# Kernel tuning notes

Measured on AMD Instinct MI355X. Metric: run time of the kernel, lower is better.

## Reference

```python
import jax, jax.numpy as jnp
import numpy as np

MIN_C, MAX_C = 1e-4, 1e4
EPS_C = 1e-6
TAU = 1.0            # fixed temperature (learnable_temperature=False), clamp is a no-op here
NORM_EPS = 1e-15
ARTANH_EPS = 1e-7

B, C, D = 512, 512, 512


def _expmap0(u, sc):
    # geoopt expmap0 for k = -c: tanh(sqrt(c)*||u||) * u / (sqrt(c)*||u||)
    norm = jnp.maximum(jnp.linalg.norm(u, axis=-1, keepdims=True), NORM_EPS)
    return jnp.tanh(sc * norm) * u / (sc * norm)


def setup_inputs() -> dict:
    key = jax.random.key(0)
    k1, k2 = jax.random.split(key)
    euclidean_feats = jax.random.normal(k1, (B, D), dtype=jnp.float32) * 0.05
    proto_tan = jax.random.normal(k2, (C, D), dtype=jnp.float32) * 0.001  # proto_init_std
    raw_c = jnp.asarray(0.0, dtype=jnp.float32)  # log(init_curvature=1.0)
    return {"euclidean_feats": euclidean_feats, "proto_tan": proto_tan, "raw_c": raw_c}


def reference(euclidean_feats, proto_tan, raw_c):
    # current_c(): softplus(raw_c) + eps, clipped
    c = jnp.clip(jax.nn.softplus(raw_c) + EPS_C, MIN_C, MAX_C)
    sc = jnp.sqrt(c)

    z = _expmap0(euclidean_feats, sc)  # (B, D) points on Poincare ball
    p = _expmap0(proto_tan, sc)        # (C, D)

    # dist(z, p) = 2/sqrt(c) * artanh(sqrt(c) * || (-z) mobius_add p ||)
    x = -z                                      # (B, D)
    x2 = jnp.sum(x * x, axis=-1)[:, None]       # (B, 1)
    y2 = jnp.sum(p * p, axis=-1)[None, :]       # (1, C)
    xy = x @ p.T                                # (B, C) inner products (GEMM)

    # mobius_add with k = -c:
    # num = (1 + 2c<x,y> + c||y||^2) x + (1 - c||x||^2) y
    # den = 1 + 2c<x,y> + c^2 ||x||^2 ||y||^2
    num = ((1.0 + 2.0 * c * xy + c * y2)[..., None] * x[:, None, :]
           + (1.0 - c * x2)[..., None] * p[None, :, :])     # (B, C, D)
    den = jnp.maximum(1.0 + 2.0 * c * xy + (c * c) * x2 * y2, NORM_EPS)  # (B, C)
    m = num / den[..., None]

    mnorm = jnp.linalg.norm(m, axis=-1)  # (B, C)
    t = jnp.clip(sc * mnorm, -1.0 + ARTANH_EPS, 1.0 - ARTANH_EPS)
    d = (2.0 / sc) * jnp.arctanh(t)      # (B, C) hyperbolic distances

    return -d / TAU
```

## Files before the change

kernel.cpp:

```cpp
#include <hip/hip_runtime.h>
#include <math.h>

#define B_ 512
#define C_ 512
#define D_ 512
#define LDK 520

typedef __attribute__((ext_vector_type(8))) short s8v;
typedef __attribute__((ext_vector_type(4))) short s4v;
typedef __attribute__((ext_vector_type(4))) float f4v;

__device__ __forceinline__ float compute_c_dev(float rc) {
    float sp = fmaxf(rc, 0.0f) + log1pf(expf(-fabsf(rc)));
    float c = sp + 1e-6f;
    return fminf(fmaxf(c, 1e-4f), 1e4f);
}

__device__ __forceinline__ unsigned short f2bf(float f) {
    unsigned u = __float_as_uint(f);
    u += 0x7FFFu + ((u >> 16) & 1u);
    return (unsigned short)(u >> 16);
}

__device__ __forceinline__ float dist_val(float zp, float x2, float y2,
                                          float c, float scc, float inv_sc) {
    float xy = -zp;
    float two_cxy = 2.0f * c * xy;
    float a = 1.0f + two_cxy + c * y2;
    float b = 1.0f - c * x2;
    float den = fmaxf(1.0f + two_cxy + c * c * x2 * y2, 1e-15f);
    float num2 = a * a * x2 + 2.0f * a * b * xy + b * b * y2;
    float mn = sqrtf(fmaxf(num2, 0.0f)) / den;
    float t = fminf(scc * mn, 1.0f - 1e-7f);
    return -inv_sc * logf((1.0f + t) / (1.0f - t));
}

__global__ __launch_bounds__(256, 1) void fused_kernel(
    const float* __restrict__ feats, const float* __restrict__ protos,
    const float* __restrict__ raw_c, float* __restrict__ out)
{
    __shared__ short zs[32 * LDK];
    __shared__ short ps[32 * LDK];
    __shared__ float x2s[32];
    __shared__ float y2s[32];

    const int t    = threadIdx.x;
    const int lane = t & 63;
    const int w    = t >> 6;
    const int row0 = blockIdx.y * 32;
    const int col0 = blockIdx.x * 32;

    const float c      = compute_c_dev(raw_c[0]);
    const float scc    = sqrtf(c);
    const float inv_sc = 1.0f / scc;

    {
        const float4* srcA = (const float4*)(feats + (size_t)(row0 + 8 * w) * D_);
        float4 v0[8], v1[8];
        #pragma unroll
        for (int i = 0; i < 8; ++i) {
            v0[i] = srcA[i * 128 + lane];
            v1[i] = srcA[i * 128 + lane + 64];
        }
        #pragma unroll
        for (int i = 0; i < 8; ++i) {
            int r = 8 * w + i;
            float ss = v0[i].x*v0[i].x + v0[i].y*v0[i].y + v0[i].z*v0[i].z + v0[i].w*v0[i].w
                     + v1[i].x*v1[i].x + v1[i].y*v1[i].y + v1[i].z*v1[i].z + v1[i].w*v1[i].w;
            #pragma unroll
            for (int off = 32; off > 0; off >>= 1) ss += __shfl_xor(ss, off);
            float n = fmaxf(sqrtf(ss), 1e-15f);
            float s = tanhf(scc * n) / (scc * n);
            if (lane == 0) x2s[r] = s * s * ss;
            s4v lo, hi;
            lo[0]=(short)f2bf(v0[i].x); lo[1]=(short)f2bf(v0[i].y);
            lo[2]=(short)f2bf(v0[i].z); lo[3]=(short)f2bf(v0[i].w);
            hi[0]=(short)f2bf(v1[i].x); hi[1]=(short)f2bf(v1[i].y);
            hi[2]=(short)f2bf(v1[i].z); hi[3]=(short)f2bf(v1[i].w);
            lo[0]=(short)f2bf(v0[i].x*s); lo[1]=(short)f2bf(v0[i].y*s);
            lo[2]=(short)f2bf(v0[i].z*s); lo[3]=(short)f2bf(v0[i].w*s);
            hi[0]=(short)f2bf(v1[i].x*s); hi[1]=(short)f2bf(v1[i].y*s);
            hi[2]=(short)f2bf(v1[i].z*s); hi[3]=(short)f2bf(v1[i].w*s);
            *(s4v*)(&zs[r * LDK + 4 * lane])       = lo;
            *(s4v*)(&zs[r * LDK + 256 + 4 * lane]) = hi;
        }
    }
    {
        const float4* srcB = (const float4*)(protos + (size_t)(col0 + 8 * w) * D_);
        float4 v0[8], v1[8];
        #pragma unroll
        for (int i = 0; i < 8; ++i) {
            v0[i] = srcB[i * 128 + lane];
            v1[i] = srcB[i * 128 + lane + 64];
        }
        #pragma unroll
        for (int i = 0; i < 8; ++i) {
            int r = 8 * w + i;
            float ss = v0[i].x*v0[i].x + v0[i].y*v0[i].y + v0[i].z*v0[i].z + v0[i].w*v0[i].w
                     + v1[i].x*v1[i].x + v1[i].y*v1[i].y + v1[i].z*v1[i].z + v1[i].w*v1[i].w;
            #pragma unroll
            for (int off = 32; off > 0; off >>= 1) ss += __shfl_xor(ss, off);
            float n = fmaxf(sqrtf(ss), 1e-15f);
            float s = tanhf(scc * n) / (scc * n);
            if (lane == 0) y2s[r] = s * s * ss;
            s4v lo, hi;
            lo[0]=(short)f2bf(v0[i].x*s); lo[1]=(short)f2bf(v0[i].y*s);
            lo[2]=(short)f2bf(v0[i].z*s); lo[3]=(short)f2bf(v0[i].w*s);
            hi[0]=(short)f2bf(v1[i].x*s); hi[1]=(short)f2bf(v1[i].y*s);
            hi[2]=(short)f2bf(v1[i].z*s); hi[3]=(short)f2bf(v1[i].w*s);
            *(s4v*)(&ps[r * LDK + 4 * lane])       = lo;
            *(s4v*)(&ps[r * LDK + 256 + 4 * lane]) = hi;
        }
    }

    __syncthreads();

    const int wr = w >> 1, wc = w & 1;
    const int rowA = 16 * wr + (lane & 15);
    const int rowB = 16 * wc + (lane & 15);
    const short* za = &zs[rowA * LDK + 8 * (lane >> 4)];
    const short* pa = &ps[rowB * LDK + 8 * (lane >> 4)];

    f4v acc = {0.f, 0.f, 0.f, 0.f};
    #pragma unroll
    for (int kk = 0; kk < 16; ++kk) {
        s8v af = *(const s8v*)(za + kk * 32);
        s8v bf = *(const s8v*)(pa + kk * 32);
        acc = __builtin_amdgcn_mfma_f32_16x16x32_bf16(af, bf, acc, 0, 0, 0);
    }

    const int col   = lane & 15;
    const int rbase = 4 * (lane >> 4);
    const int gcol  = col0 + 16 * wc + col;
    const float y2  = y2s[16 * wc + col];
    #pragma unroll
    for (int r = 0; r < 4; ++r) {
        int lrow = 16 * wr + rbase + r;
        float x2 = x2s[lrow];
        out[(size_t)(row0 + lrow) * C_ + gcol] = dist_val(acc[r], x2, y2, c, scc, inv_sc);
    }
}

extern "C" void kernel_launch(void* const* d_in, const int* in_sizes, int n_in,
                              void* d_out, int out_size, void* d_ws, size_t ws_size,
                              hipStream_t stream) {
    const float* feats  = (const float*)d_in[0];
    const float* protos = (const float*)d_in[1];
    const float* raw_c  = (const float*)d_in[2];
    float* out = (float*)d_out;

    dim3 grid(C_ / 32, B_ / 32);
    fused_kernel<<<grid, 256, 0, stream>>>(feats, protos, raw_c, out);
}
```

Before: 66.62 us.

## Double block size, load A/B tiles in parallel, split-K MFMA across wave halves

Raises the block from 256 to 512 threads. Waves 0-3 now load and normalize the feature tile while waves 4-7 handle the prototype tile at the same time, instead of one wave group doing both in sequence. The K dimension of the MFMA loop is split between the two wave halves and reduced through shared memory, which adds one extra barrier. It also switches to fast intrinsics for tanh, division and log, and removes the dead first bf16 conversion pass, trading some accuracy for shorter transcendental paths.

New measurement: 63.62 us. -4.5%, faster.

```diff
diff --git a/kernel.cpp b/kernel.cpp
--- a/kernel.cpp
+++ b/kernel.cpp
@@ -22,6 +22,11 @@
     return (unsigned short)(u >> 16);
 }
 
+__device__ __forceinline__ float fast_tanh_pos(float x) {
+    float e = __expf(2.0f * x);
+    return 1.0f - __fdividef(2.0f, e + 1.0f);
+}
+
 __device__ __forceinline__ float dist_val(float zp, float x2, float y2,
                                           float c, float scc, float inv_sc) {
     float xy = -zp;
@@ -30,12 +35,12 @@
     float b = 1.0f - c * x2;
     float den = fmaxf(1.0f + two_cxy + c * c * x2 * y2, 1e-15f);
     float num2 = a * a * x2 + 2.0f * a * b * xy + b * b * y2;
-    float mn = sqrtf(fmaxf(num2, 0.0f)) / den;
+    float mn = __fdividef(sqrtf(fmaxf(num2, 0.0f)), den);
     float t = fminf(scc * mn, 1.0f - 1e-7f);
-    return -inv_sc * logf((1.0f + t) / (1.0f - t));
+    return -inv_sc * __logf(__fdividef(1.0f + t, 1.0f - t));
 }
 
-__global__ __launch_bounds__(256, 1) void fused_kernel(
+__global__ __launch_bounds__(512, 2) void fused_kernel(
     const float* __restrict__ feats, const float* __restrict__ protos,
     const float* __restrict__ raw_c, float* __restrict__ out)
 {
@@ -43,6 +48,7 @@
     __shared__ short ps[32 * LDK];
     __shared__ float x2s[32];
     __shared__ float y2s[32];
+    __shared__ f4v  accbuf[256];
 
     const int t    = threadIdx.x;
     const int lane = t & 63;
@@ -55,89 +61,74 @@
     const float inv_sc = 1.0f / scc;
 
     {
-        const float4* srcA = (const float4*)(feats + (size_t)(row0 + 8 * w) * D_);
+        const bool  isB = (w >= 4);
+        const int   wl  = isB ? (w - 4) : w;
+        const float* src = isB ? (protos + (size_t)(col0 + 8 * wl) * D_)
+                               : (feats  + (size_t)(row0 + 8 * wl) * D_);
+        short* dst = isB ? ps : zs;
+        float* sqv = isB ? y2s : x2s;
+
+        const float4* s4 = (const float4*)src;
         float4 v0[8], v1[8];
         #pragma unroll
         for (int i = 0; i < 8; ++i) {
-            v0[i] = srcA[i * 128 + lane];
-            v1[i] = srcA[i * 128 + lane + 64];
+            v0[i] = s4[i * 128 + lane];
+            v1[i] = s4[i * 128 + lane + 64];
         }
         #pragma unroll
         for (int i = 0; i < 8; ++i) {
-            int r = 8 * w + i;
+            int r = 8 * wl + i;
             float ss = v0[i].x*v0[i].x + v0[i].y*v0[i].y + v0[i].z*v0[i].z + v0[i].w*v0[i].w
                      + v1[i].x*v1[i].x + v1[i].y*v1[i].y + v1[i].z*v1[i].z + v1[i].w*v1[i].w;
             #pragma unroll
             for (int off = 32; off > 0; off >>= 1) ss += __shfl_xor(ss, off);
             float n = fmaxf(sqrtf(ss), 1e-15f);
-            float s = tanhf(scc * n) / (scc * n);
-            if (lane == 0) x2s[r] = s * s * ss;
-            s4v lo, hi;
-            lo[0]=(short)f2bf(v0[i].x); lo[1]=(short)f2bf(v0[i].y);
-            lo[2]=(short)f2bf(v0[i].z); lo[3]=(short)f2bf(v0[i].w);
-            hi[0]=(short)f2bf(v1[i].x); hi[1]=(short)f2bf(v1[i].y);
-            hi[2]=(short)f2bf(v1[i].z); hi[3]=(short)f2bf(v1[i].w);
-            lo[0]=(short)f2bf(v0[i].x*s); lo[1]=(short)f2bf(v0[i].y*s);
-            lo[2]=(short)f2bf(v0[i].z*s); lo[3]=(short)f2bf(v0[i].w*s);
-            hi[0]=(short)f2bf(v1[i].x*s); hi[1]=(short)f2bf(v1[i].y*s);
-            hi[2]=(short)f2bf(v1[i].z*s); hi[3]=(short)f2bf(v1[i].w*s);
-            *(s4v*)(&zs[r * LDK + 4 * lane])       = lo;
-            *(s4v*)(&zs[r * LDK + 256 + 4 * lane]) = hi;
-        }
-    }
-    {
-        const float4* srcB = (const float4*)(protos + (size_t)(col0 + 8 * w) * D_);
-        float4 v0[8], v1[8];
-        #pragma unroll
-        for (int i = 0; i < 8; ++i) {
-            v0[i] = srcB[i * 128 + lane];
-            v1[i] = srcB[i * 128 + lane + 64];
-        }
-        #pragma unroll
-        for (int i = 0; i < 8; ++i) {
-            int r = 8 * w + i;
-            float ss = v0[i].x*v0[i].x + v0[i].y*v0[i].y + v0[i].z*v0[i].z + v0[i].w*v0[i].w
-                     + v1[i].x*v1[i].x + v1[i].y*v1[i].y + v1[i].z*v1[i].z + v1[i].w*v1[i].w;
-            #pragma unroll
-            for (int off = 32; off > 0; off >>= 1) ss += __shfl_xor(ss, off);
-            float n = fmaxf(sqrtf(ss), 1e-15f);
-            float s = tanhf(scc * n) / (scc * n);
-            if (lane == 0) y2s[r] = s * s * ss;
+            float arg = scc * n;
+            float s = __fdividef(fast_tanh_pos(arg), arg);
+            if (lane == 0) sqv[r] = s * s * ss;
             s4v lo, hi;
             lo[0]=(short)f2bf(v0[i].x*s); lo[1]=(short)f2bf(v0[i].y*s);
             lo[2]=(short)f2bf(v0[i].z*s); lo[3]=(short)f2bf(v0[i].w*s);
             hi[0]=(short)f2bf(v1[i].x*s); hi[1]=(short)f2bf(v1[i].y*s);
             hi[2]=(short)f2bf(v1[i].z*s); hi[3]=(short)f2bf(v1[i].w*s);
-            *(s4v*)(&ps[r * LDK + 4 * lane])       = lo;
-            *(s4v*)(&ps[r * LDK + 256 + 4 * lane]) = hi;
+            *(s4v*)(&dst[r * LDK + 4 * lane])       = lo;
+            *(s4v*)(&dst[r * LDK + 256 + 4 * lane]) = hi;
         }
     }
 
     __syncthreads();
 
-    const int wr = w >> 1, wc = w & 1;
+    const int q     = w & 3;
+    const int khalf = w >> 2;
+    const int wr = q >> 1, wc = q & 1;
     const int rowA = 16 * wr + (lane & 15);
     const int rowB = 16 * wc + (lane & 15);
-    const short* za = &zs[rowA * LDK + 8 * (lane >> 4)];
-    const short* pa = &ps[rowB * LDK + 8 * (lane >> 4)];
+    const short* za = &zs[rowA * LDK + 8 * (lane >> 4) + khalf * 256];
+    const short* pa = &ps[rowB * LDK + 8 * (lane >> 4) + khalf * 256];
 
     f4v acc = {0.f, 0.f, 0.f, 0.f};
     #pragma unroll
-    for (int kk = 0; kk < 16; ++kk) {
+    for (int kk = 0; kk < 8; ++kk) {
         s8v af = *(const s8v*)(za + kk * 32);
         s8v bf = *(const s8v*)(pa + kk * 32);
         acc = __builtin_amdgcn_mfma_f32_16x16x32_bf16(af, bf, acc, 0, 0, 0);
     }
 
-    const int col   = lane & 15;
-    const int rbase = 4 * (lane >> 4);
-    const int gcol  = col0 + 16 * wc + col;
-    const float y2  = y2s[16 * wc + col];
-    #pragma unroll
-    for (int r = 0; r < 4; ++r) {
-        int lrow = 16 * wr + rbase + r;
-        float x2 = x2s[lrow];
-        out[(size_t)(row0 + lrow) * C_ + gcol] = dist_val(acc[r], x2, y2, c, scc, inv_sc);
+    if (khalf) accbuf[q * 64 + lane] = acc;
+    __syncthreads();
+
+    if (!khalf) {
+        acc += accbuf[q * 64 + lane];
+        const int col   = lane & 15;
+        const int rbase = 4 * (lane >> 4);
+        const int gcol  = col0 + 16 * wc + col;
+        const float y2  = y2s[16 * wc + col];
+        #pragma unroll
+        for (int r = 0; r < 4; ++r) {
+            int lrow = 16 * wr + rbase + r;
+            float x2 = x2s[lrow];
+            out[(size_t)(row0 + lrow) * C_ + gcol] = dist_val(acc[r], x2, y2, c, scc, inv_sc);
+        }
     }
 }
 
@@ -150,5 +141,5 @@
     float* out = (float*)d_out;
 
     dim3 grid(C_ / 32, B_ / 32);
-    fused_kernel<<<grid, 256, 0, stream>>>(feats, protos, raw_c, out);
+    fused_kernel<<<grid, 512, 0, stream>>>(feats, protos, raw_c, out);
 }
```
